# Optimization experiments

Hardware: AMD Instinct MI355X
Metric: run time of the kernel (lower is better)

## Reference

```python
import jax, jax.numpy as jnp
import numpy as np

ALPHA = 0.2  # LeakyReLU negative slope
NEG_INF = -9e15


def setup_inputs() -> dict:
    key = jax.random.key(0)
    ks = jax.random.split(key, 6)
    B, N, F_in, F_out = 16, 1024, 1024, 512
    x = jax.random.normal(ks[0], (B, N, F_in), dtype=jnp.float32)
    adj = jax.random.randint(ks[1], (B, N, N), 0, 2, dtype=jnp.int32)
    W = jax.random.normal(ks[2], (F_in, F_out), dtype=jnp.float32) * 0.02
    a = jax.random.normal(ks[3], (2 * F_out, 1), dtype=jnp.float32) * 0.02
    fc_w = jax.random.normal(ks[4], (F_out, 2 * F_out), dtype=jnp.float32) * 0.02
    fc_b = jnp.zeros((F_out,), dtype=jnp.float32)
    return {"x": x, "adj": adj, "W": W, "a": a, "fc_w": fc_w, "fc_b": fc_b}


def reference(x, adj, W, a, fc_w, fc_b):
    # h: [B, N, F_out]
    h = jnp.matmul(x, W)
    F_out = W.shape[1]
    # The original builds a_input = concat(h_i, h_j) of shape [B,N,N,2F] and
    # contracts with a. Equivalently (same math, no O(N^2 F) intermediate):
    # e_ij = leakyrelu(h_i . a[:F] + h_j . a[F:])
    a1 = a[:F_out, 0]  # [F_out]
    a2 = a[F_out:, 0]  # [F_out]
    f1 = jnp.einsum('bnf,f->bn', h, a1)  # source term
    f2 = jnp.einsum('bnf,f->bn', h, a2)  # target term
    e = jax.nn.leaky_relu(f1[:, :, None] + f2[:, None, :], negative_slope=ALPHA)  # [B,N,N]
    attention = jnp.where(adj > 0, e, jnp.full_like(e, NEG_INF))
    attention = jax.nn.softmax(attention, axis=2)
    # dropout is identity in eval mode
    agg = jnp.matmul(attention, h)  # [B,N,F_out]
    h_prime = jnp.concatenate([agg, h], axis=2)  # [B,N,2F]
    h_prime = jnp.matmul(h_prime, fc_w.T) + fc_b
    return jax.nn.elu(h_prime)  # concat=True path
```

## Files before the change

### kernel.cpp

```cpp
#include <hip/hip_runtime.h>

#define ALPHA 0.2f

typedef __attribute__((ext_vector_type(8))) short short8;
typedef __attribute__((ext_vector_type(4))) float f32x4;

__device__ __forceinline__ unsigned short f2b(float f) {
  unsigned int u; __builtin_memcpy(&u, &f, 4);
  unsigned int r = (u + 0x7FFFu + ((u >> 16) & 1u)) >> 16;
  return (unsigned short)r;
}
__device__ __forceinline__ float b2f(unsigned short v) {
  unsigned int u = ((unsigned int)v) << 16; float f; __builtin_memcpy(&f, &u, 4); return f;
}
__device__ __forceinline__ void gl_lds16(const unsigned short* g, unsigned short* l) {
  __builtin_amdgcn_global_load_lds((__attribute__((address_space(1))) void*)g,
                                   (__attribute__((address_space(3))) void*)l, 16, 0, 0);
}
__device__ __forceinline__ uint4 pack8(float4 v0, float4 v1) {
  alignas(16) unsigned short o[8];
  o[0] = f2b(v0.x); o[1] = f2b(v0.y); o[2] = f2b(v0.z); o[3] = f2b(v0.w);
  o[4] = f2b(v1.x); o[5] = f2b(v1.y); o[6] = f2b(v1.z); o[7] = f2b(v1.w);
  return *(const uint4*)o;
}
__device__ __forceinline__ void vm8() { asm volatile("s_waitcnt vmcnt(8)" ::: "memory"); }
__device__ __forceinline__ void vm6() { asm volatile("s_waitcnt vmcnt(6)" ::: "memory"); }
__device__ __forceinline__ void vm4() { asm volatile("s_waitcnt vmcnt(4)" ::: "memory"); }
__device__ __forceinline__ void vm0() { asm volatile("s_waitcnt vmcnt(0)" ::: "memory"); }
__device__ __forceinline__ void lg0() { asm volatile("s_waitcnt lgkmcnt(0)" ::: "memory"); }

__device__ __forceinline__ void cvt_f4(const float* __restrict__ in,
                                       unsigned short* __restrict__ out,
                                       unsigned int f4idx) {
  float4 v = ((const float4*)in)[f4idx];
  alignas(8) unsigned short o[4];
  o[0] = f2b(v.x); o[1] = f2b(v.y); o[2] = f2b(v.z); o[3] = f2b(v.w);
  ((uint2*)out)[f4idx] = *(const uint2*)o;
}

__global__ __launch_bounds__(256) void prep1(const float* __restrict__ fcw,
                                             unsigned short* __restrict__ fcwb,
                                             const float* __restrict__ W,
                                             unsigned short* __restrict__ Wt) {
  __shared__ alignas(16) unsigned short tile[64][72];
  unsigned int bx = blockIdx.x;
  unsigned int tid = threadIdx.x;
  if (bx < 256u) {
    unsigned int base = bx * 512u;
    cvt_f4(fcw, fcwb, base + tid);
    cvt_f4(fcw, fcwb, base + 256u + tid);
  } else {
    unsigned int idx = bx - 256u;
    unsigned int k0 = (idx >> 3) * 64, n0 = (idx & 7) * 64;
    #pragma unroll
    for (int p = 0; p < 4; p++) {
      int r = p * 16 + (tid >> 4);
      int c = (tid & 15) * 4;
      float4 v = *(const float4*)(W + (size_t)(k0 + r) * 512 + n0 + c);
      tile[r][c] = f2b(v.x); tile[r][c + 1] = f2b(v.y);
      tile[r][c + 2] = f2b(v.z); tile[r][c + 3] = f2b(v.w);
    }
    __syncthreads();
    int f = tid >> 2;
    int ic = (tid & 3) * 16;
    alignas(16) unsigned short buf[16];
    #pragma unroll
    for (int k = 0; k < 16; k++) buf[k] = tile[ic + k][f];
    uint4* dst = (uint4*)(Wt + (size_t)(n0 + f) * 1024 + k0 + ic);
    dst[0] = ((const uint4*)buf)[0];
    dst[1] = ((const uint4*)buf)[1];
  }
}

__global__ __launch_bounds__(256) void prep2(const unsigned short* __restrict__ hp,
                                             const float* __restrict__ a,
                                             float* __restrict__ f1, float* __restrict__ f2) {
  int row = blockIdx.x * 4 + (threadIdx.x >> 6);
  int lane = threadIdx.x & 63;
  const unsigned short* hrow = hp + (size_t)row * 1024 + 512;
  uint4 raw = *(const uint4*)(hrow + lane * 8);
  alignas(16) unsigned short hv[8]; __builtin_memcpy(hv, &raw, 16);
  float s1 = 0.f, s2 = 0.f;
  #pragma unroll
  for (int j = 0; j < 8; j++) {
    float hf = b2f(hv[j]);
    s1 += hf * a[lane * 8 + j];
    s2 += hf * a[512 + lane * 8 + j];
  }
  #pragma unroll
  for (int o = 32; o > 0; o >>= 1) { s1 += __shfl_down(s1, o); s2 += __shfl_down(s2, o); }
  if (lane == 0) { f1[row] = s1; f2[row] = s2; }
}

__global__ __launch_bounds__(256) void rowsum_P(const int* __restrict__ adj,
                                                const float* __restrict__ f1,
                                                const float* __restrict__ f2,
                                                float* __restrict__ invl,
                                                unsigned short* __restrict__ P) {
  int row = blockIdx.x * 4 + (threadIdx.x >> 6);
  int lane = threadIdx.x & 63;
  int b = row >> 10;
  float f1v = f1[row];
  const int4* ap = (const int4*)(adj + (size_t)row * 1024) + lane * 4;
  int4 a0 = ap[0];
  int4 a1 = ap[1];
  int4 a2 = ap[2];
  int4 a3 = ap[3];
  int av[16] = {a0.x, a0.y, a0.z, a0.w, a1.x, a1.y, a1.z, a1.w,
                a2.x, a2.y, a2.z, a2.w, a3.x, a3.y, a3.z, a3.w};
  const float* f2p = f2 + (b << 10) + lane * 16;
  float4 v0 = ((const float4*)f2p)[0];
  float4 v1 = ((const float4*)f2p)[1];
  float4 v2 = ((const float4*)f2p)[2];
  float4 v3 = ((const float4*)f2p)[3];
  float fv[16] = {v0.x, v0.y, v0.z, v0.w, v1.x, v1.y, v1.z, v1.w,
                  v2.x, v2.y, v2.z, v2.w, v3.x, v3.y, v3.z, v3.w};
  float s = 0.f;
  alignas(16) unsigned short o[16];
  #pragma unroll
  for (int j = 0; j < 16; j++) {
    float p = 0.f;
    if (av[j] > 0) {
      float z = f1v + fv[j];
      z = z > 0.f ? z : ALPHA * z;
      p = __expf(z);
      s += p;
    }
    o[j] = f2b(p);
  }
  uint4* dst = (uint4*)(P + (size_t)row * 1024 + lane * 16);
  dst[0] = ((const uint4*)o)[0];
  dst[1] = ((const uint4*)o)[1];
  #pragma unroll
  for (int off = 32; off > 0; off >>= 1) s += __shfl_down(s, off);
  if (lane == 0) invl[row] = 1.0f / s;
}

template <int EPI, int CVTA>
__global__ __launch_bounds__(512, 2) void gemm_bt(
    const void* __restrict__ A_, size_t aBS,
    const unsigned short* __restrict__ Bt, size_t bBS,
    int K,
    void* __restrict__ outp, size_t oBS, int ldo, int ocol,
    const float* __restrict__ scale,
    const float* __restrict__ bias,
    unsigned short* __restrict__ htout) {
  __shared__ alignas(16) unsigned short smem[49152];
  unsigned short* As = smem;
  unsigned short* Bs = smem + 16384;
  const int tid = threadIdx.x;
  const int lane = tid & 63;
  const int w = tid >> 6;
  const int m0 = blockIdx.x * 128;
  const int n0 = blockIdx.y * 256;
  const int zb = blockIdx.z;
  const unsigned short* Btb = Bt + (size_t)zb * bBS;

  f32x4 acc[4][4];
  #pragma unroll
  for (int i = 0; i < 4; i++)
    #pragma unroll
    for (int j = 0; j < 4; j++)
      #pragma unroll
      for (int r = 0; r < 4; r++) acc[i][j][r] = 0.f;

  const int lr = lane >> 3;
  const int lc = (lane & 7) ^ lr;
  const unsigned short* ag = nullptr;
  const float* agf = nullptr;
  if (CVTA)
    agf = (const float*)A_ + (size_t)(m0 + w * 8 + lr) * K + lc * 8;
  else
    ag = (const unsigned short*)A_ + (size_t)zb * aBS + (size_t)(m0 + w * 8 + lr) * K + lc * 8;
  const unsigned short* bg = Btb + (size_t)(n0 + w * 8 + lr) * K + lc * 8;
  const int asb = w * 512;
  const int bsb = w * 512;
  const int aw = asb + lane * 8;

  const int wm = (w & 1) * 64;
  const int wn = (w >> 1) * 64;
  const int row16 = lane & 15;
  const int quad = lane >> 4;
  const int sw = row16 & 7;

  const int nk = K >> 6;

  if (CVTA) {
    float4 a0[2][2], a1[2][2];
    #pragma unroll
    for (int t = 0; t < 2; t++) {
      a0[t][0] = *(const float4*)(agf + (size_t)(t * 64) * K);
      a0[t][1] = *(const float4*)(agf + (size_t)(t * 64) * K + 4);
    }
    #pragma unroll
    for (int t = 0; t < 4; t++)
      gl_lds16(bg + (size_t)(t * 64) * K, Bs + t * 4096 + bsb);
    #pragma unroll
    for (int t = 0; t < 2; t++) {
      a1[t][0] = *(const float4*)(agf + 64 + (size_t)(t * 64) * K);
      a1[t][1] = *(const float4*)(agf + 64 + (size_t)(t * 64) * K + 4);
    }
    #pragma unroll
    for (int t = 0; t < 4; t++)
      gl_lds16(bg + 64 + (size_t)(t * 64) * K, Bs + 16384 + t * 4096 + bsb);
    vm8();
    #pragma unroll
    for (int t = 0; t < 2; t++)
      *(uint4*)(As + t * 4096 + aw) = pack8(a0[t][0], a0[t][1]);
    vm4();
    #pragma unroll
    for (int t = 0; t < 2; t++)
      *(uint4*)(As + 8192 + t * 4096 + aw) = pack8(a1[t][0], a1[t][1]);
  } else {
    #pragma unroll
    for (int t = 0; t < 2; t++)
      gl_lds16(ag + (size_t)(t * 64) * K, As + t * 4096 + asb);
    #pragma unroll
    for (int t = 0; t < 4; t++)
      gl_lds16(bg + (size_t)(t * 64) * K, Bs + t * 4096 + bsb);
    #pragma unroll
    for (int t = 0; t < 2; t++)
      gl_lds16(ag + 64 + (size_t)(t * 64) * K, As + 8192 + t * 4096 + asb);
    #pragma unroll
    for (int t = 0; t < 4; t++)
      gl_lds16(bg + 64 + (size_t)(t * 64) * K, Bs + 16384 + t * 4096 + bsb);
    vm6();
  }
  lg0();
  __builtin_amdgcn_s_barrier();

  for (int k = 0; k < nk; k++) {
    const int ab = (k & 1) * 8192;
    const int bb = (k & 1) * 16384;
    const bool st2 = (k + 2 < nk);
    const bool pub = (k + 1 < nk);

    short8 af[2][4], bf[2][4];
    #pragma unroll
    for (int s = 0; s < 2; s++) {
      #pragma unroll
      for (int i = 0; i < 4; i++) {
        af[s][i] = *(const short8*)(As + ab + (wm + i * 16 + row16) * 64 + ((s * 4 + quad) ^ sw) * 8);
        bf[s][i] = *(const short8*)(Bs + bb + (wn + i * 16 + row16) * 64 + ((s * 4 + quad) ^ sw) * 8);
      }
    }
    lg0();
    __builtin_amdgcn_s_barrier();

    float4 av[2][2];
    if (st2) {
      const int ko = (k + 2) * 64;
      if (CVTA) {
        #pragma unroll
        for (int t = 0; t < 2; t++) {
          av[t][0] = *(const float4*)(agf + ko + (size_t)(t * 64) * K);
          av[t][1] = *(const float4*)(agf + ko + (size_t)(t * 64) * K + 4);
        }
      } else {
        #pragma unroll
        for (int t = 0; t < 2; t++)
          gl_lds16(ag + ko + (size_t)(t * 64) * K, As + ab + t * 4096 + asb);
      }
      #pragma unroll
      for (int t = 0; t < 4; t++)
        gl_lds16(bg + ko + (size_t)(t * 64) * K, Bs + bb + t * 4096 + bsb);
    }

    __builtin_amdgcn_s_setprio(1);
    #pragma unroll
    for (int s = 0; s < 2; s++)
      #pragma unroll
      for (int am = 0; am < 4; am++)
        #pragma unroll
        for (int bn = 0; bn < 4; bn++)
          acc[am][bn] = __builtin_amdgcn_mfma_f32_16x16x32_bf16(af[s][am], bf[s][bn], acc[am][bn], 0, 0, 0);
    __builtin_amdgcn_s_setprio(0);

    if (pub) {
      if (CVTA) {
        if (st2) {
          vm4();
          #pragma unroll
          for (int t = 0; t < 2; t++)
            *(uint4*)(As + ab + t * 4096 + aw) = pack8(av[t][0], av[t][1]);
        } else {
          vm0();
        }
        lg0();
      } else {
        if (st2) vm6(); else vm0();
      }
      __builtin_amdgcn_s_barrier();
    }
  }

  const int col = lane & 15;
  const int r0 = quad * 4;
  #pragma unroll
  for (int am = 0; am < 4; am++) {
    #pragma unroll
    for (int bn = 0; bn < 4; bn++) {
      #pragma unroll
      for (int r = 0; r < 4; r++) {
        int m = m0 + wm + am * 16 + r0 + r;
        int n = n0 + wn + bn * 16 + col;
        float v = acc[am][bn][r];
        if (EPI == 3) v *= scale[zb * 1024 + m];
        if (EPI == 2) {
          v += bias[n];
          v = v > 0.f ? v : expm1f(v);
          ((float*)outp)[(size_t)m * ldo + n] = v;
        } else {
          ((unsigned short*)outp)[(size_t)zb * oBS + (size_t)m * ldo + ocol + n] = f2b(v);
        }
      }
    }
  }

  if (EPI == 1) {
    __syncthreads();
    #pragma unroll
    for (int am = 0; am < 4; am++)
      #pragma unroll
      for (int bn = 0; bn < 4; bn++)
        #pragma unroll
        for (int r = 0; r < 4; r++) {
          int mloc = wm + am * 16 + r0 + r;
          int nloc = wn + bn * 16 + col;
          smem[nloc * 136 + mloc] = f2b(acc[am][bn][r]);
        }
    __syncthreads();
    const int b = m0 >> 10;
    const int i0 = m0 & 1023;
    unsigned short* htp = htout + ((size_t)(b * 512 + n0) << 10) + i0;
    #pragma unroll
    for (int p = 0; p < 8; p++) {
      int f = p * 32 + (tid >> 4);
      int ib = (tid & 15) * 8;
      uint4 v = *(const uint4*)(smem + f * 136 + ib);
      *(uint4*)(htp + ((size_t)f << 10) + ib) = v;
    }
  }
}

extern "C" void kernel_launch(void* const* d_in, const int* in_sizes, int n_in,
                              void* d_out, int out_size, void* d_ws, size_t ws_size,
                              hipStream_t stream) {
  const float* x   = (const float*)d_in[0];
  const int*   adj = (const int*)d_in[1];
  const float* W   = (const float*)d_in[2];
  const float* a   = (const float*)d_in[3];
  const float* fcw = (const float*)d_in[4];
  const float* fcb = (const float*)d_in[5];
  float* out = (float*)d_out;
  char* ws = (char*)d_ws;

  unsigned short* P    = (unsigned short*)(ws);
  unsigned short* hp   = (unsigned short*)(ws + 33554432);
  unsigned short* ht   = (unsigned short*)(ws + 67108864);
  unsigned short* Wt   = (unsigned short*)(ws + 83886080);
  unsigned short* fcwb = (unsigned short*)(ws + 84934656);
  float* f1            = (float*)(ws + 85983232);
  float* f2            = (float*)(ws + 86048768);
  float* invl          = (float*)(ws + 86114304);

  prep1<<<384, 256, 0, stream>>>(fcw, fcwb, W, Wt);

  gemm_bt<1, 1><<<dim3(128, 2, 1), 512, 0, stream>>>(x, 0, Wt, 0, 1024,
                                                     hp, 0, 1024, 512, nullptr, nullptr, ht);
  prep2<<<4096, 256, 0, stream>>>(hp, a, f1, f2);
  rowsum_P<<<4096, 256, 0, stream>>>(adj, f1, f2, invl, P);

  gemm_bt<3, 0><<<dim3(8, 2, 16), 512, 0, stream>>>(P, 1024 * 1024, ht, 512 * 1024, 1024,
                                                    hp, 1024 * 1024, 1024, 0, invl, nullptr, nullptr);
  gemm_bt<2, 0><<<dim3(128, 2, 1), 512, 0, stream>>>(hp, 0, fcwb, 0, 1024,
                                                     out, 0, 512, 0, nullptr, fcb, nullptr);
}
```

Baseline: 259.5 us.

## Fuse attention projections into first GEMM epilogue and single-buffer GEMM LDS

Removes the prep2 kernel. The f1/f2 dot products with `a` are now computed in the epilogue of the x·W GEMM, using shuffle reductions, LDS atomics and global atomicAdd into buffers zeroed by an extra prep1 block. The GEMM also drops from double-buffered to single-buffered LDS (halving shared memory) and raises launch bounds to 4 blocks per CU. This trades the two-stage prefetch pipeline for higher occupancy. It also adds float atomics, which make the f1/f2 summation order nondeterministic.

```diff
diff --git a/kernel.cpp b/kernel.cpp
--- a/kernel.cpp
+++ b/kernel.cpp
@@ -23,11 +23,6 @@
   o[4] = f2b(v1.x); o[5] = f2b(v1.y); o[6] = f2b(v1.z); o[7] = f2b(v1.w);
   return *(const uint4*)o;
 }
-__device__ __forceinline__ void vm8() { asm volatile("s_waitcnt vmcnt(8)" ::: "memory"); }
-__device__ __forceinline__ void vm6() { asm volatile("s_waitcnt vmcnt(6)" ::: "memory"); }
-__device__ __forceinline__ void vm4() { asm volatile("s_waitcnt vmcnt(4)" ::: "memory"); }
-__device__ __forceinline__ void vm0() { asm volatile("s_waitcnt vmcnt(0)" ::: "memory"); }
-__device__ __forceinline__ void lg0() { asm volatile("s_waitcnt lgkmcnt(0)" ::: "memory"); }
 
 __device__ __forceinline__ void cvt_f4(const float* __restrict__ in,
                                        unsigned short* __restrict__ out,
@@ -41,7 +36,9 @@
 __global__ __launch_bounds__(256) void prep1(const float* __restrict__ fcw,
                                              unsigned short* __restrict__ fcwb,
                                              const float* __restrict__ W,
-                                             unsigned short* __restrict__ Wt) {
+                                             unsigned short* __restrict__ Wt,
+                                             float* __restrict__ f1z,
+                                             float* __restrict__ f2z) {
   __shared__ alignas(16) unsigned short tile[64][72];
   unsigned int bx = blockIdx.x;
   unsigned int tid = threadIdx.x;
@@ -49,7 +46,7 @@
     unsigned int base = bx * 512u;
     cvt_f4(fcw, fcwb, base + tid);
     cvt_f4(fcw, fcwb, base + 256u + tid);
-  } else {
+  } else if (bx < 384u) {
     unsigned int idx = bx - 256u;
     unsigned int k0 = (idx >> 3) * 64, n0 = (idx & 7) * 64;
     #pragma unroll
@@ -69,27 +66,13 @@
     uint4* dst = (uint4*)(Wt + (size_t)(n0 + f) * 1024 + k0 + ic);
     dst[0] = ((const uint4*)buf)[0];
     dst[1] = ((const uint4*)buf)[1];
-  }
-}
-
-__global__ __launch_bounds__(256) void prep2(const unsigned short* __restrict__ hp,
-                                             const float* __restrict__ a,
-                                             float* __restrict__ f1, float* __restrict__ f2) {
-  int row = blockIdx.x * 4 + (threadIdx.x >> 6);
-  int lane = threadIdx.x & 63;
-  const unsigned short* hrow = hp + (size_t)row * 1024 + 512;
-  uint4 raw = *(const uint4*)(hrow + lane * 8);
-  alignas(16) unsigned short hv[8]; __builtin_memcpy(hv, &raw, 16);
-  float s1 = 0.f, s2 = 0.f;
-  #pragma unroll
-  for (int j = 0; j < 8; j++) {
-    float hf = b2f(hv[j]);
-    s1 += hf * a[lane * 8 + j];
-    s2 += hf * a[512 + lane * 8 + j];
-  }
-  #pragma unroll
-  for (int o = 32; o > 0; o >>= 1) { s1 += __shfl_down(s1, o); s2 += __shfl_down(s2, o); }
-  if (lane == 0) { f1[row] = s1; f2[row] = s2; }
+  } else {
+    float4 z = {0.f, 0.f, 0.f, 0.f};
+    #pragma unroll
+    for (int i = 0; i < 16; i++) ((float4*)f1z)[i * 256 + tid] = z;
+    #pragma unroll
+    for (int i = 0; i < 16; i++) ((float4*)f2z)[i * 256 + tid] = z;
+  }
 }
 
 __global__ __launch_bounds__(256) void rowsum_P(const int* __restrict__ adj,
@@ -137,17 +120,18 @@
 }
 
 template <int EPI, int CVTA>
-__global__ __launch_bounds__(512, 2) void gemm_bt(
+__global__ __launch_bounds__(512, 4) void gemm_bt(
     const void* __restrict__ A_, size_t aBS,
     const unsigned short* __restrict__ Bt, size_t bBS,
     int K,
     void* __restrict__ outp, size_t oBS, int ldo, int ocol,
     const float* __restrict__ scale,
     const float* __restrict__ bias,
-    unsigned short* __restrict__ htout) {
-  __shared__ alignas(16) unsigned short smem[49152];
+    unsigned short* __restrict__ htout,
+    float* __restrict__ f1g, float* __restrict__ f2g) {
+  __shared__ alignas(16) unsigned short smem[24576];
   unsigned short* As = smem;
-  unsigned short* Bs = smem + 16384;
+  unsigned short* Bs = smem + 8192;
   const int tid = threadIdx.x;
   const int lane = tid & 63;
   const int w = tid >> 6;
@@ -173,83 +157,55 @@
   else
     ag = (const unsigned short*)A_ + (size_t)zb * aBS + (size_t)(m0 + w * 8 + lr) * K + lc * 8;
   const unsigned short* bg = Btb + (size_t)(n0 + w * 8 + lr) * K + lc * 8;
-  const int asb = w * 512;
-  const int bsb = w * 512;
-  const int aw = asb + lane * 8;
+  const int sb = w * 512;
+  const int aw = sb + lane * 8;
 
   const int wm = (w & 1) * 64;
   const int wn = (w >> 1) * 64;
   const int row16 = lane & 15;
   const int quad = lane >> 4;
   const int sw = row16 & 7;
-
   const int nk = K >> 6;
 
   if (CVTA) {
-    float4 a0[2][2], a1[2][2];
+    float4 av[2][2];
     #pragma unroll
     for (int t = 0; t < 2; t++) {
-      a0[t][0] = *(const float4*)(agf + (size_t)(t * 64) * K);
-      a0[t][1] = *(const float4*)(agf + (size_t)(t * 64) * K + 4);
+      av[t][0] = *(const float4*)(agf + (size_t)(t * 64) * K);
+      av[t][1] = *(const float4*)(agf + (size_t)(t * 64) * K + 4);
     }
     #pragma unroll
     for (int t = 0; t < 4; t++)
-      gl_lds16(bg + (size_t)(t * 64) * K, Bs + t * 4096 + bsb);
-    #pragma unroll
-    for (int t = 0; t < 2; t++) {
-      a1[t][0] = *(const float4*)(agf + 64 + (size_t)(t * 64) * K);
-      a1[t][1] = *(const float4*)(agf + 64 + (size_t)(t * 64) * K + 4);
-    }
+      gl_lds16(bg + (size_t)(t * 64) * K, Bs + t * 4096 + sb);
+    #pragma unroll
+    for (int t = 0; t < 2; t++)
+      *(uint4*)(As + t * 4096 + aw) = pack8(av[t][0], av[t][1]);
+  } else {
+    #pragma unroll
+    for (int t = 0; t < 2; t++)
+      gl_lds16(ag + (size_t)(t * 64) * K, As + t * 4096 + sb);
     #pragma unroll
     for (int t = 0; t < 4; t++)
-      gl_lds16(bg + 64 + (size_t)(t * 64) * K, Bs + 16384 + t * 4096 + bsb);
-    vm8();
-    #pragma unroll
-    for (int t = 0; t < 2; t++)
-      *(uint4*)(As + t * 4096 + aw) = pack8(a0[t][0], a0[t][1]);
-    vm4();
-    #pragma unroll
-    for (int t = 0; t < 2; t++)
-      *(uint4*)(As + 8192 + t * 4096 + aw) = pack8(a1[t][0], a1[t][1]);
-  } else {
-    #pragma unroll
-    for (int t = 0; t < 2; t++)
-      gl_lds16(ag + (size_t)(t * 64) * K, As + t * 4096 + asb);
-    #pragma unroll
-    for (int t = 0; t < 4; t++)
-      gl_lds16(bg + (size_t)(t * 64) * K, Bs + t * 4096 + bsb);
-    #pragma unroll
-    for (int t = 0; t < 2; t++)
-      gl_lds16(ag + 64 + (size_t)(t * 64) * K, As + 8192 + t * 4096 + asb);
-    #pragma unroll
-    for (int t = 0; t < 4; t++)
-      gl_lds16(bg + 64 + (size_t)(t * 64) * K, Bs + 16384 + t * 4096 + bsb);
-    vm6();
-  }
-  lg0();
-  __builtin_amdgcn_s_barrier();
+      gl_lds16(bg + (size_t)(t * 64) * K, Bs + t * 4096 + sb);
+  }
+  __syncthreads();
 
   for (int k = 0; k < nk; k++) {
-    const int ab = (k & 1) * 8192;
-    const int bb = (k & 1) * 16384;
-    const bool st2 = (k + 2 < nk);
-    const bool pub = (k + 1 < nk);
-
     short8 af[2][4], bf[2][4];
     #pragma unroll
     for (int s = 0; s < 2; s++) {
       #pragma unroll
       for (int i = 0; i < 4; i++) {
-        af[s][i] = *(const short8*)(As + ab + (wm + i * 16 + row16) * 64 + ((s * 4 + quad) ^ sw) * 8);
-        bf[s][i] = *(const short8*)(Bs + bb + (wn + i * 16 + row16) * 64 + ((s * 4 + quad) ^ sw) * 8);
-      }
-    }
-    lg0();
-    __builtin_amdgcn_s_barrier();
-
+        af[s][i] = *(const short8*)(As + (wm + i * 16 + row16) * 64 + ((s * 4 + quad) ^ sw) * 8);
+        bf[s][i] = *(const short8*)(Bs + (wn + i * 16 + row16) * 64 + ((s * 4 + quad) ^ sw) * 8);
+      }
+    }
+    __syncthreads();
+
+    const bool st = (k + 1 < nk);
     float4 av[2][2];
-    if (st2) {
-      const int ko = (k + 2) * 64;
+    if (st) {
+      const int ko = (k + 1) * 64;
       if (CVTA) {
         #pragma unroll
         for (int t = 0; t < 2; t++) {
@@ -259,14 +215,13 @@
       } else {
         #pragma unroll
         for (int t = 0; t < 2; t++)
-          gl_lds16(ag + ko + (size_t)(t * 64) * K, As + ab + t * 4096 + asb);
+          gl_lds16(ag + ko + (size_t)(t * 64) * K, As + t * 4096 + sb);
       }
       #pragma unroll
       for (int t = 0; t < 4; t++)
-        gl_lds16(bg + ko + (size_t)(t * 64) * K, Bs + bb + t * 4096 + bsb);
-    }
-
-    __builtin_amdgcn_s_setprio(1);
+        gl_lds16(bg + ko + (size_t)(t * 64) * K, Bs + t * 4096 + sb);
+    }
+
     #pragma unroll
     for (int s = 0; s < 2; s++)
       #pragma unroll
@@ -274,24 +229,13 @@
         #pragma unroll
         for (int bn = 0; bn < 4; bn++)
           acc[am][bn] = __builtin_amdgcn_mfma_f32_16x16x32_bf16(af[s][am], bf[s][bn], acc[am][bn], 0, 0, 0);
-    __builtin_amdgcn_s_setprio(0);
-
-    if (pub) {
-      if (CVTA) {
-        if (st2) {
-          vm4();
-          #pragma unroll
-          for (int t = 0; t < 2; t++)
-            *(uint4*)(As + ab + t * 4096 + aw) = pack8(av[t][0], av[t][1]);
-        } else {
-          vm0();
-        }
-        lg0();
-      } else {
-        if (st2) vm6(); else vm0();
-      }
-      __builtin_amdgcn_s_barrier();
-    }
+
+    if (st && CVTA) {
+      #pragma unroll
+      for (int t = 0; t < 2; t++)
+        *(uint4*)(As + t * 4096 + aw) = pack8(av[t][0], av[t][1]);
+    }
+    __syncthreads();
   }
 
   const int col = lane & 15;
@@ -318,27 +262,79 @@
   }
 
   if (EPI == 1) {
-    __syncthreads();
+    float* fbuf = (float*)smem;
+    if (tid < 256) fbuf[tid] = 0.f;
+    __syncthreads();
+    float a1v[4], a2v[4];
+    #pragma unroll
+    for (int bn = 0; bn < 4; bn++) {
+      int n = n0 + wn + bn * 16 + col;
+      a1v[bn] = scale[n];
+      a2v[bn] = scale[512 + n];
+    }
+    float p1[16], p2[16];
     #pragma unroll
     for (int am = 0; am < 4; am++)
       #pragma unroll
-      for (int bn = 0; bn < 4; bn++)
+      for (int r = 0; r < 4; r++) {
+        float s1 = 0.f, s2 = 0.f;
+        #pragma unroll
+        for (int bn = 0; bn < 4; bn++) {
+          float hb = b2f(f2b(acc[am][bn][r]));
+          s1 += hb * a1v[bn];
+          s2 += hb * a2v[bn];
+        }
+        p1[am * 4 + r] = s1;
+        p2[am * 4 + r] = s2;
+      }
+    #pragma unroll
+    for (int mask = 1; mask < 16; mask <<= 1)
+      #pragma unroll
+      for (int e = 0; e < 16; e++) {
+        p1[e] += __shfl_xor(p1[e], mask);
+        p2[e] += __shfl_xor(p2[e], mask);
+      }
+    if ((lane & 15) == 0) {
+      #pragma unroll
+      for (int am = 0; am < 4; am++)
         #pragma unroll
         for (int r = 0; r < 4; r++) {
-          int mloc = wm + am * 16 + r0 + r;
-          int nloc = wn + bn * 16 + col;
-          smem[nloc * 136 + mloc] = f2b(acc[am][bn][r]);
+          int ml = wm + am * 16 + r0 + r;
+          atomicAdd(&fbuf[ml], p1[am * 4 + r]);
+          atomicAdd(&fbuf[128 + ml], p2[am * 4 + r]);
         }
-    __syncthreads();
+    }
+    __syncthreads();
+    if (tid < 128) atomicAdd(&f1g[m0 + tid], fbuf[tid]);
+    else if (tid < 256) atomicAdd(&f2g[m0 + tid - 128], fbuf[tid]);
+    __syncthreads();
+
     const int b = m0 >> 10;
     const int i0 = m0 & 1023;
-    unsigned short* htp = htout + ((size_t)(b * 512 + n0) << 10) + i0;
-    #pragma unroll
-    for (int p = 0; p < 8; p++) {
-      int f = p * 32 + (tid >> 4);
-      int ib = (tid & 15) * 8;
-      uint4 v = *(const uint4*)(smem + f * 136 + ib);
-      *(uint4*)(htp + ((size_t)f << 10) + ib) = v;
+    #pragma unroll
+    for (int pass = 0; pass < 2; pass++) {
+      if ((wn >> 7) == pass) {
+        int nl = wn & 127;
+        #pragma unroll
+        for (int am = 0; am < 4; am++)
+          #pragma unroll
+          for (int bn = 0; bn < 4; bn++)
+            #pragma unroll
+            for (int r = 0; r < 4; r++) {
+              int nloc = nl + bn * 16 + col;
+              int mloc = wm + am * 16 + r0 + r;
+              smem[nloc * 136 + mloc] = f2b(acc[am][bn][r]);
+            }
+      }
+      __syncthreads();
+      #pragma unroll
+      for (int p = 0; p < 4; p++) {
+        int fr = p * 32 + (tid >> 4);
+        int ib = (tid & 15) * 8;
+        uint4 v = *(const uint4*)(smem + fr * 136 + ib);
+        *(uint4*)(htout + ((size_t)(b * 512 + n0 + pass * 128 + fr) << 10) + i0 + ib) = v;
+      }
+      __syncthreads();
     }
   }
 }
@@ -364,15 +360,17 @@
   float* f2            = (float*)(ws + 86048768);
   float* invl          = (float*)(ws + 86114304);
 
-  prep1<<<384, 256, 0, stream>>>(fcw, fcwb, W, Wt);
+  prep1<<<385, 256, 0, stream>>>(fcw, fcwb, W, Wt, f1, f2);
 
   gemm_bt<1, 1><<<dim3(128, 2, 1), 512, 0, stream>>>(x, 0, Wt, 0, 1024,
-                                                     hp, 0, 1024, 512, nullptr, nullptr, ht);
-  prep2<<<4096, 256, 0, stream>>>(hp, a, f1, f2);
+                                                     hp, 0, 1024, 512, a, nullptr,
+                                                     ht, f1, f2);
   rowsum_P<<<4096, 256, 0, stream>>>(adj, f1, f2, invl, P);
 
   gemm_bt<3, 0><<<dim3(8, 2, 16), 512, 0, stream>>>(P, 1024 * 1024, ht, 512 * 1024, 1024,
-                                                    hp, 1024 * 1024, 1024, 0, invl, nullptr, nullptr);
+                                                    hp, 1024 * 1024, 1024, 0, invl, nullptr,
+                                                    nullptr, nullptr, nullptr);
   gemm_bt<2, 0><<<dim3(128, 2, 1), 512, 0, stream>>>(hp, 0, fcwb, 0, 1024,
-                                                     out, 0, 512, 0, nullptr, fcb, nullptr);
-}
+                                                     out, 0, 512, 0, nullptr, fcb,
+                                                     nullptr, nullptr, nullptr);
+}
```

Measured after the change: 574.3 us. 2.21x slower.
